# Kernel tuning notes

Measured on AMD Instinct MI355X. Metric: run time of the kernel, lower is better.

The kernel has to match this reference:

```python
import jax, jax.numpy as jnp
import numpy as np

B, S, H = 32, 2048, 512

def setup_inputs() -> dict:
    key = jax.random.key(0)
    k1, k2, k3, k4 = jax.random.split(key, 4)
    Y = jax.random.normal(k1, (B, S, H), dtype=jnp.float32)
    mask_Y = jnp.ones((B, S), dtype=jnp.float32)
    W = jax.random.normal(k2, (H, H), dtype=jnp.float32)
    b = jax.random.normal(k3, (H,), dtype=jnp.float32)
    w = jax.random.normal(k4, (H,), dtype=jnp.float32)
    return {"Y": Y, "mask_Y": mask_Y, "W": W, "b": b, "w": w}

def reference(Y, mask_Y, W, b, w):
    # u: [B,S,H] = tanh(Y @ W + b)
    u = jnp.tanh(jnp.einsum('bsh,hd->bsd', Y, W) + b)
    # scores: [B,S] = u . w, masked with large negative additive bias
    scores = jnp.einsum('bsh,h->bs', u, w) - 1000.0 * (1.0 - mask_Y)
    alpha = jax.nn.softmax(scores, axis=1)  # [B,S]
    # c_star: [B,H] = attention-weighted sum of Y
    c_star = jnp.einsum('bs,bsh->bh', alpha, Y)
    return c_star
```

## Files before the change

### kernel.cpp

```cpp
#include <hip/hip_runtime.h>
#include <hip/hip_bf16.h>


#define Bsz 32
#define Ssz 2048
#define Hsz 512
#define Msz (Bsz * Ssz)

using half8   = __attribute__((ext_vector_type(8))) _Float16;
using floatx4 = __attribute__((ext_vector_type(4))) float;

__device__ __forceinline__ void llds(_Float16* l, const _Float16* g) {
  __builtin_amdgcn_global_load_lds((const __attribute__((address_space(1))) void*)g,
                                   (__attribute__((address_space(3))) void*)l, 16, 0, 0);
}

__device__ __forceinline__ float fast_tanh(float x) {
  const float e = __expf(2.f * x);
  return 1.f - 2.f / (e + 1.f);
}

__global__ __launch_bounds__(256) void wsplit_k(const float* __restrict__ W,
                                                _Float16* __restrict__ Wt) {
  __shared__ float tile[32][33];
  const int bx = blockIdx.x & 15, by = blockIdx.x >> 4;
  const int tx = threadIdx.x & 31, ty = threadIdx.x >> 5;
#pragma unroll
  for (int i = 0; i < 4; ++i)
    tile[ty + 8 * i][tx] = W[(size_t)(by * 32 + ty + 8 * i) * Hsz + bx * 32 + tx];
  __syncthreads();
#pragma unroll
  for (int i = 0; i < 4; ++i) {
    const int n = bx * 32 + ty + 8 * i;
    const int k = by * 32 + tx;
    Wt[(size_t)n * Hsz + k] = (_Float16)tile[tx][ty + 8 * i];
  }
}

__global__ __launch_bounds__(256) void gemm_score_k(const float* __restrict__ Y,
                                                    const _Float16* __restrict__ Wt,
                                                    const float* __restrict__ bvec,
                                                    const float* __restrict__ wvec,
                                                    float* __restrict__ scores4) {
  __shared__ __align__(16) _Float16 As[128 * 32];
  __shared__ __align__(16) _Float16 Bh[128 * 32];
  const int tid = threadIdx.x;
  const int lane = tid & 63, wv = tid >> 6;
  const int wr = wv >> 1, wc = wv & 1;
  const int lr = lane & 15, lq = lane >> 4;
  const int g = blockIdx.x;
  const int x = g & 7, q = g >> 3;
  const int nblk = q & 3;
  const int mblk = (q >> 2) * 8 + x;

  floatx4 acc[4][4];
#pragma unroll
  for (int rf = 0; rf < 4; ++rf)
#pragma unroll
    for (int cf = 0; cf < 4; ++cf)
      acc[rf][cf] = (floatx4){0.f, 0.f, 0.f, 0.f};

  const int arow = tid >> 1;
  const int p0 = (tid & 1) * 2;
  const float* aga = Y + ((size_t)(mblk * 128 + arow)) * Hsz + p0 * 8;
  const int s0 = (p0 ^ ((arow >> 1) & 3)) * 8;
  const int s1 = ((p0 + 1) ^ ((arow >> 1) & 3)) * 8;
  const size_t brow0 = (size_t)nblk * 128 * Hsz;

  const int bc = wv * 64 + lane;
  const int brow_a = bc >> 1;
  for (int it = 0; it < 16; ++it) {
    const int k0 = it * 32;
#pragma unroll
    for (int i = 0; i < 2; ++i) {
      const int c = i * 256 + wv * 64 + lane;
      const int brow = c >> 2;
      const int gpart = (c & 3) ^ ((c >> 3) & 3);
      llds(&Bh[(i * 256 + wv * 64) * 8],
           Wt + brow0 + (size_t)brow * Hsz + (k0 + gpart * 8));
    }
    {
      const float4* g4 = (const float4*)(aga + k0);
      const float4 f0 = g4[0], f1 = g4[1], f2 = g4[2], f3 = g4[3];
      half8 h0, h1;
      h0[0] = (_Float16)f0.x; h0[1] = (_Float16)f0.y; h0[2] = (_Float16)f0.z; h0[3] = (_Float16)f0.w;
      h0[4] = (_Float16)f1.x; h0[5] = (_Float16)f1.y; h0[6] = (_Float16)f1.z; h0[7] = (_Float16)f1.w;
      h1[0] = (_Float16)f2.x; h1[1] = (_Float16)f2.y; h1[2] = (_Float16)f2.z; h1[3] = (_Float16)f2.w;
      h1[4] = (_Float16)f3.x; h1[5] = (_Float16)f3.y; h1[6] = (_Float16)f3.z; h1[7] = (_Float16)f3.w;
      *(half8*)&As[arow * 32 + s0] = h0;
      *(half8*)&As[arow * 32 + s1] = h1;
    }
    __syncthreads();

    half8 a[4], bhf[4];
#pragma unroll
    for (int rf = 0; rf < 4; ++rf) {
      const int ar = wr * 64 + rf * 16 + lr;
      a[rf] = *(const half8*)&As[ar * 32 + (lq ^ ((ar >> 1) & 3)) * 8];
    }
#pragma unroll
    for (int cf = 0; cf < 4; ++cf) {
      const int nr = wc * 64 + cf * 16 + lr;
      bhf[cf] = *(const half8*)&Bh[nr * 32 + (lq ^ ((nr >> 1) & 3)) * 8];
    }
#pragma unroll
    for (int rf = 0; rf < 4; ++rf)
#pragma unroll
      for (int cf = 0; cf < 4; ++cf)
        acc[rf][cf] = __builtin_amdgcn_mfma_f32_16x16x32_f16(a[rf], bhf[cf], acc[rf][cf], 0, 0, 0);
    __syncthreads();
  }

  float bb[4], ww[4];
  const int colbase = nblk * 128 + wc * 64;
#pragma unroll
  for (int cf = 0; cf < 4; ++cf) {
    const int col = colbase + cf * 16 + lr;
    bb[cf] = bvec[col];
    ww[cf] = wvec[col];
  }
  float* red = (float*)As;
#pragma unroll
  for (int rf = 0; rf < 4; ++rf) {
#pragma unroll
    for (int r = 0; r < 4; ++r) {
      float v = 0.f;
#pragma unroll
      for (int cf = 0; cf < 4; ++cf)
        v += fast_tanh(acc[rf][cf][r] + bb[cf]) * ww[cf];
      v += __shfl_xor(v, 1, 16);
      v += __shfl_xor(v, 2, 16);
      v += __shfl_xor(v, 4, 16);
      v += __shfl_xor(v, 8, 16);
      if (lr == 0)
        red[(wr * 64 + rf * 16 + lq * 4 + r) * 2 + wc] = v;
    }
  }
  __syncthreads();
  if (tid < 128)
    scores4[(size_t)nblk * Msz + mblk * 128 + tid] = red[2 * tid] + red[2 * tid + 1];
}

__global__ __launch_bounds__(256) void softmax_k(const float* __restrict__ scores4,
                                                 const float* __restrict__ mask,
                                                 float* __restrict__ alpha) {
  const int b = blockIdx.x, t = threadIdx.x;
  const int lane = t & 63, wv = t >> 6;
  float s[8];
  float mx = -3.4e38f;
#pragma unroll
  for (int i = 0; i < 8; ++i) {
    const int idx = b * Ssz + i * 256 + t;
    float v = scores4[idx] + scores4[Msz + idx] + scores4[2 * Msz + idx] + scores4[3 * Msz + idx];
    v -= 1000.f * (1.f - mask[idx]);
    s[i] = v;
    mx = fmaxf(mx, v);
  }
  for (int off = 32; off > 0; off >>= 1) mx = fmaxf(mx, __shfl_xor(mx, off, 64));
  __shared__ float rm[4], rs[4];
  if (lane == 0) rm[wv] = mx;
  __syncthreads();
  mx = fmaxf(fmaxf(rm[0], rm[1]), fmaxf(rm[2], rm[3]));
  float sum = 0.f;
#pragma unroll
  for (int i = 0; i < 8; ++i) {
    s[i] = __expf(s[i] - mx);
    sum += s[i];
  }
  for (int off = 32; off > 0; off >>= 1) sum += __shfl_xor(sum, off, 64);
  if (lane == 0) rs[wv] = sum;
  __syncthreads();
  sum = rs[0] + rs[1] + rs[2] + rs[3];
  const float inv = 1.f / sum;
#pragma unroll
  for (int i = 0; i < 8; ++i) alpha[b * Ssz + i * 256 + t] = s[i] * inv;
}

__global__ __launch_bounds__(256) void wsum1_k(const float* __restrict__ alpha,
                                               const float* __restrict__ Y,
                                               float* __restrict__ partial) {
  const int b = blockIdx.x >> 5, sc = blockIdx.x & 31;
  const int t = threadIdx.x, lane = t & 63, wv = t >> 6;
  __shared__ float part[4 * 512];
  const int s0 = sc * 64 + wv * 16;
  const float* al = alpha + b * Ssz + s0;
  const float4* Yb = (const float4*)(Y + ((size_t)b * Ssz + s0) * Hsz);
  float a0 = 0.f, a1 = 0.f, a2 = 0.f, a3 = 0.f, a4 = 0.f, a5 = 0.f, a6 = 0.f, a7 = 0.f;
#pragma unroll 4
  for (int r = 0; r < 16; ++r) {
    const float a = al[r];
    const float4 y0 = Yb[r * 128 + lane * 2];
    const float4 y1 = Yb[r * 128 + lane * 2 + 1];
    a0 = fmaf(a, y0.x, a0); a1 = fmaf(a, y0.y, a1);
    a2 = fmaf(a, y0.z, a2); a3 = fmaf(a, y0.w, a3);
    a4 = fmaf(a, y1.x, a4); a5 = fmaf(a, y1.y, a5);
    a6 = fmaf(a, y1.z, a6); a7 = fmaf(a, y1.w, a7);
  }
  part[wv * 512 + 0 * 64 + lane] = a0;
  part[wv * 512 + 1 * 64 + lane] = a1;
  part[wv * 512 + 2 * 64 + lane] = a2;
  part[wv * 512 + 3 * 64 + lane] = a3;
  part[wv * 512 + 4 * 64 + lane] = a4;
  part[wv * 512 + 5 * 64 + lane] = a5;
  part[wv * 512 + 6 * 64 + lane] = a6;
  part[wv * 512 + 7 * 64 + lane] = a7;
  __syncthreads();
#pragma unroll
  for (int i = 0; i < 2; ++i) {
    const int h = i * 256 + t;
    const int idx = (h & 7) * 64 + (h >> 3);
    partial[((size_t)(b * 32 + sc)) * Hsz + h] =
        part[idx] + part[512 + idx] + part[1024 + idx] + part[1536 + idx];
  }
}

__global__ __launch_bounds__(256) void wsum2_k(const float* __restrict__ partial,
                                               float* __restrict__ out) {
  const int b = blockIdx.x >> 1;
  const int h = (blockIdx.x & 1) * 256 + threadIdx.x;
  float s = 0.f;
#pragma unroll 8
  for (int sc = 0; sc < 32; ++sc)
    s += partial[((size_t)(b * 32 + sc)) * Hsz + h];
  out[b * Hsz + h] = s;
}

extern "C" void kernel_launch(void* const* d_in, const int* in_sizes, int n_in,
                              void* d_out, int out_size, void* d_ws, size_t ws_size,
                              hipStream_t stream) {
  (void)in_sizes; (void)n_in; (void)out_size; (void)ws_size;
  const float* Y    = (const float*)d_in[0];
  const float* mask = (const float*)d_in[1];
  const float* W    = (const float*)d_in[2];
  const float* bvec = (const float*)d_in[3];
  const float* wvec = (const float*)d_in[4];
  float* out = (float*)d_out;

  char* ws = (char*)d_ws;
  _Float16* Wt   = (_Float16*)ws;
  float* scores4 = (float*)(ws + ((size_t)1 << 20));
  float* alpha   = (float*)(ws + ((size_t)2 << 20));
  float* partial = (float*)(ws + ((size_t)2 << 20) + (512u << 10));

  wsplit_k<<<256, 256, 0, stream>>>(W, Wt);
  gemm_score_k<<<(Msz / 128) * 4, 256, 0, stream>>>(Y, Wt, bvec, wvec, scores4);
  softmax_k<<<Bsz, 256, 0, stream>>>(scores4, mask, alpha);
  wsum1_k<<<Bsz * 32, 256, 0, stream>>>(alpha, Y, partial);
  wsum2_k<<<Bsz * 2, 256, 0, stream>>>(partial, out);
}
```

Measured before the change: 274.4 us.

## Retile score GEMM to full-N 32-row blocks, removing N-split partial scores

The score GEMM now gives each block 32 rows of Y against all 512 columns of W, where before it used 128x128 tiles split four ways along N. Y is therefore read and converted to fp16 once instead of four times, and only one score array is written, so softmax no longer sums four partials. The loop also prefetches the next Y slice into registers while running MFMAs. The cost is a 32KB B tile that every block restages from L2 each k-step, and lower MFMA arithmetic intensity per LDS load.

```diff
diff --git a/kernel.cpp b/kernel.cpp
--- a/kernel.cpp
+++ b/kernel.cpp
@@ -8,6 +8,7 @@
 #define Msz (Bsz * Ssz)
 
 using half8   = __attribute__((ext_vector_type(8))) _Float16;
+using half4   = __attribute__((ext_vector_type(4))) _Float16;
 using floatx4 = __attribute__((ext_vector_type(4))) float;
 
 __device__ __forceinline__ void llds(_Float16* l, const _Float16* g) {
@@ -41,107 +42,106 @@
                                                     const _Float16* __restrict__ Wt,
                                                     const float* __restrict__ bvec,
                                                     const float* __restrict__ wvec,
-                                                    float* __restrict__ scores4) {
-  __shared__ __align__(16) _Float16 As[128 * 32];
-  __shared__ __align__(16) _Float16 Bh[128 * 32];
+                                                    float* __restrict__ scores) {
+  __shared__ __align__(16) _Float16 As[32 * 32];
+  __shared__ __align__(16) _Float16 Bs[512 * 32];
   const int tid = threadIdx.x;
   const int lane = tid & 63, wv = tid >> 6;
-  const int wr = wv >> 1, wc = wv & 1;
   const int lr = lane & 15, lq = lane >> 4;
-  const int g = blockIdx.x;
-  const int x = g & 7, q = g >> 3;
-  const int nblk = q & 3;
-  const int mblk = (q >> 2) * 8 + x;
-
-  floatx4 acc[4][4];
-#pragma unroll
-  for (int rf = 0; rf < 4; ++rf)
-#pragma unroll
-    for (int cf = 0; cf < 4; ++cf)
+  const int mblk = blockIdx.x;
+
+  floatx4 acc[2][8];
+#pragma unroll
+  for (int rf = 0; rf < 2; ++rf)
+#pragma unroll
+    for (int cf = 0; cf < 8; ++cf)
       acc[rf][cf] = (floatx4){0.f, 0.f, 0.f, 0.f};
 
-  const int arow = tid >> 1;
-  const int p0 = (tid & 1) * 2;
-  const float* aga = Y + ((size_t)(mblk * 128 + arow)) * Hsz + p0 * 8;
-  const int s0 = (p0 ^ ((arow >> 1) & 3)) * 8;
-  const int s1 = ((p0 + 1) ^ ((arow >> 1) & 3)) * 8;
-  const size_t brow0 = (size_t)nblk * 128 * Hsz;
-
-  const int bc = wv * 64 + lane;
-  const int brow_a = bc >> 1;
+  const int arow = tid >> 3, aseg = tid & 7;
+  const float* aga = Y + ((size_t)(mblk * 32 + arow)) * Hsz + aseg * 4;
+  const int aslot = (aseg >> 1) ^ ((arow >> 1) & 3);
+  const int awoff = arow * 32 + aslot * 8 + (aseg & 1) * 4;
+
+  auto stageB = [&](int it) {
+    const int k0 = it * 32;
+#pragma unroll
+    for (int i = 0; i < 8; ++i) {
+      const int cbase = i * 256 + wv * 64;
+      const int c = cbase + lane;
+      const int brow = c >> 2;
+      const int gpart = (c & 3) ^ ((brow >> 1) & 3);
+      llds(&Bs[cbase * 8], Wt + (size_t)brow * Hsz + (k0 + gpart * 8));
+    }
+  };
+  auto writeA = [&](const float4 f) {
+    half4 h;
+    h[0] = (_Float16)f.x; h[1] = (_Float16)f.y;
+    h[2] = (_Float16)f.z; h[3] = (_Float16)f.w;
+    *(half4*)&As[awoff] = h;
+  };
+
+  float4 fa = *(const float4*)aga;
+  stageB(0);
+  writeA(fa);
+  __syncthreads();
+
   for (int it = 0; it < 16; ++it) {
-    const int k0 = it * 32;
-#pragma unroll
-    for (int i = 0; i < 2; ++i) {
-      const int c = i * 256 + wv * 64 + lane;
-      const int brow = c >> 2;
-      const int gpart = (c & 3) ^ ((c >> 3) & 3);
-      llds(&Bh[(i * 256 + wv * 64) * 8],
-           Wt + brow0 + (size_t)brow * Hsz + (k0 + gpart * 8));
-    }
-    {
-      const float4* g4 = (const float4*)(aga + k0);
-      const float4 f0 = g4[0], f1 = g4[1], f2 = g4[2], f3 = g4[3];
-      half8 h0, h1;
-      h0[0] = (_Float16)f0.x; h0[1] = (_Float16)f0.y; h0[2] = (_Float16)f0.z; h0[3] = (_Float16)f0.w;
-      h0[4] = (_Float16)f1.x; h0[5] = (_Float16)f1.y; h0[6] = (_Float16)f1.z; h0[7] = (_Float16)f1.w;
-      h1[0] = (_Float16)f2.x; h1[1] = (_Float16)f2.y; h1[2] = (_Float16)f2.z; h1[3] = (_Float16)f2.w;
-      h1[4] = (_Float16)f3.x; h1[5] = (_Float16)f3.y; h1[6] = (_Float16)f3.z; h1[7] = (_Float16)f3.w;
-      *(half8*)&As[arow * 32 + s0] = h0;
-      *(half8*)&As[arow * 32 + s1] = h1;
-    }
-    __syncthreads();
-
-    half8 a[4], bhf[4];
-#pragma unroll
-    for (int rf = 0; rf < 4; ++rf) {
-      const int ar = wr * 64 + rf * 16 + lr;
+    half8 a[2];
+#pragma unroll
+    for (int rf = 0; rf < 2; ++rf) {
+      const int ar = rf * 16 + lr;
       a[rf] = *(const half8*)&As[ar * 32 + (lq ^ ((ar >> 1) & 3)) * 8];
     }
-#pragma unroll
-    for (int cf = 0; cf < 4; ++cf) {
-      const int nr = wc * 64 + cf * 16 + lr;
-      bhf[cf] = *(const half8*)&Bh[nr * 32 + (lq ^ ((nr >> 1) & 3)) * 8];
-    }
-#pragma unroll
-    for (int rf = 0; rf < 4; ++rf)
-#pragma unroll
-      for (int cf = 0; cf < 4; ++cf)
-        acc[rf][cf] = __builtin_amdgcn_mfma_f32_16x16x32_f16(a[rf], bhf[cf], acc[rf][cf], 0, 0, 0);
-    __syncthreads();
-  }
-
-  float bb[4], ww[4];
-  const int colbase = nblk * 128 + wc * 64;
-#pragma unroll
-  for (int cf = 0; cf < 4; ++cf) {
-    const int col = colbase + cf * 16 + lr;
+    if (it < 15)
+      fa = *(const float4*)(aga + (it + 1) * 32);
+
+#pragma unroll
+    for (int cf = 0; cf < 8; ++cf) {
+      const int nr = wv * 128 + cf * 16 + lr;
+      const half8 b = *(const half8*)&Bs[nr * 32 + (lq ^ ((nr >> 1) & 3)) * 8];
+      acc[0][cf] = __builtin_amdgcn_mfma_f32_16x16x32_f16(a[0], b, acc[0][cf], 0, 0, 0);
+      acc[1][cf] = __builtin_amdgcn_mfma_f32_16x16x32_f16(a[1], b, acc[1][cf], 0, 0, 0);
+    }
+    if (it < 15) {
+      __syncthreads();
+      stageB(it + 1);
+      writeA(fa);
+      __syncthreads();
+    }
+  }
+
+  float bb[8], ww[8];
+#pragma unroll
+  for (int cf = 0; cf < 8; ++cf) {
+    const int col = wv * 128 + cf * 16 + lr;
     bb[cf] = bvec[col];
     ww[cf] = wvec[col];
   }
+  __syncthreads();
   float* red = (float*)As;
 #pragma unroll
-  for (int rf = 0; rf < 4; ++rf) {
+  for (int rf = 0; rf < 2; ++rf) {
 #pragma unroll
     for (int r = 0; r < 4; ++r) {
       float v = 0.f;
 #pragma unroll
-      for (int cf = 0; cf < 4; ++cf)
+      for (int cf = 0; cf < 8; ++cf)
         v += fast_tanh(acc[rf][cf][r] + bb[cf]) * ww[cf];
       v += __shfl_xor(v, 1, 16);
       v += __shfl_xor(v, 2, 16);
       v += __shfl_xor(v, 4, 16);
       v += __shfl_xor(v, 8, 16);
       if (lr == 0)
-        red[(wr * 64 + rf * 16 + lq * 4 + r) * 2 + wc] = v;
-    }
-  }
-  __syncthreads();
-  if (tid < 128)
-    scores4[(size_t)nblk * Msz + mblk * 128 + tid] = red[2 * tid] + red[2 * tid + 1];
-}
-
-__global__ __launch_bounds__(256) void softmax_k(const float* __restrict__ scores4,
+        red[(rf * 16 + lq * 4 + r) * 4 + wv] = v;
+    }
+  }
+  __syncthreads();
+  if (tid < 32)
+    scores[mblk * 32 + tid] =
+        red[tid * 4] + red[tid * 4 + 1] + red[tid * 4 + 2] + red[tid * 4 + 3];
+}
+
+__global__ __launch_bounds__(256) void softmax_k(const float* __restrict__ scores,
                                                  const float* __restrict__ mask,
                                                  float* __restrict__ alpha) {
   const int b = blockIdx.x, t = threadIdx.x;
@@ -151,8 +151,7 @@
 #pragma unroll
   for (int i = 0; i < 8; ++i) {
     const int idx = b * Ssz + i * 256 + t;
-    float v = scores4[idx] + scores4[Msz + idx] + scores4[2 * Msz + idx] + scores4[3 * Msz + idx];
-    v -= 1000.f * (1.f - mask[idx]);
+    float v = scores[idx] - 1000.f * (1.f - mask[idx]);
     s[i] = v;
     mx = fmaxf(mx, v);
   }
@@ -238,13 +237,13 @@
 
   char* ws = (char*)d_ws;
   _Float16* Wt   = (_Float16*)ws;
-  float* scores4 = (float*)(ws + ((size_t)1 << 20));
-  float* alpha   = (float*)(ws + ((size_t)2 << 20));
-  float* partial = (float*)(ws + ((size_t)2 << 20) + (512u << 10));
+  float* scores  = (float*)(ws + ((size_t)1 << 20));
+  float* alpha   = (float*)(ws + ((size_t)1 << 20) + (256u << 10));
+  float* partial = (float*)(ws + ((size_t)2 << 20));
 
   wsplit_k<<<256, 256, 0, stream>>>(W, Wt);
-  gemm_score_k<<<(Msz / 128) * 4, 256, 0, stream>>>(Y, Wt, bvec, wvec, scores4);
-  softmax_k<<<Bsz, 256, 0, stream>>>(scores4, mask, alpha);
+  gemm_score_k<<<Msz / 32, 256, 0, stream>>>(Y, Wt, bvec, wvec, scores);
+  softmax_k<<<Bsz, 256, 0, stream>>>(scores, mask, alpha);
   wsum1_k<<<Bsz * 32, 256, 0, stream>>>(alpha, Y, partial);
   wsum2_k<<<Bsz * 2, 256, 0, stream>>>(partial, out);
 }
```

Result: slower. 289.4 us (+5.5%).
